# Optimization experiments

Hardware: AMD Instinct MI355X
Metric: run time of the kernel (lower is better)

Reference implementation:

```python
import jax, jax.numpy as jnp
import numpy as np

NEG = -1e30  # mask value safe for logsumexp/max
HALF_POS = 4   # positive window: [t-4, t+4)
HALF_ALL = 16  # combined window: [t-16, t+16) (pos + 12 negatives each side)


def _normalize(x, axis=-1, eps=1e-12):
    # matches torch F.normalize: x / max(||x||, eps)
    n = jnp.linalg.norm(x, axis=axis, keepdims=True)
    return x / jnp.maximum(n, eps)


def _banded_logits(q, k, temperature):
    # q, k: [B, T, D] (normalized). Returns logits [B, T, W], valid mask, pos mask.
    B, T, D = q.shape
    offsets = jnp.arange(-HALF_ALL, HALF_ALL)          # [W=32]
    j = jnp.arange(T)[:, None] + offsets[None, :]      # [T, W] absolute indices
    valid = (j >= 0) & (j < T)                         # combined (pos+neg) window
    jc = jnp.clip(j, 0, T - 1)
    kg = k[:, jc, :]                                   # [B, T, W, D]
    logits = jnp.einsum('btd,btwd->btw', q, kg) / temperature
    pos = valid & (offsets >= -HALF_POS)[None, :] & (offsets < HALF_POS)[None, :]
    return logits, valid, pos


def _direction(q, k, temperature):
    logits, valid, pos = _banded_logits(q, k, temperature)
    lse_all = jax.nn.logsumexp(jnp.where(valid, logits, NEG), axis=2)  # [B, T]
    lse_pos = jax.nn.logsumexp(jnp.where(pos, logits, NEG), axis=2)    # [B, T]
    # per-t loss is mean over batch; summed over t
    loss_sum = jnp.sum(jnp.mean(lse_all - lse_pos, axis=0))
    max_all = jnp.max(jnp.where(valid, logits, NEG), axis=2)
    max_pos = jnp.max(jnp.where(pos, logits, NEG), axis=2)
    # argmax falls in positive block (positives listed first -> ties go positive)
    correct = jnp.sum((max_pos >= max_all).astype(jnp.float32))
    return loss_sum, correct


def setup_inputs() -> dict:
    key = jax.random.key(0)
    k1, k2 = jax.random.split(key)
    B, T, D = 16, 4096, 128
    return {
        'motion_feature': jax.random.normal(k1, (B, T, D), dtype=jnp.float32),
        'audio_feature': jax.random.normal(k2, (B, T, D), dtype=jnp.float32),
    }


def reference(motion_feature, audio_feature):
    temperature = 0.1
    B, T, D = motion_feature.shape
    m = _normalize(motion_feature, axis=2)
    a = _normalize(audio_feature, axis=2)
    m2a_loss, m2a_correct = _direction(m, a, temperature)
    a2m_loss, a2m_correct = _direction(a, m, temperature)
    final_loss = (m2a_loss + a2m_loss) / (2 * T)
    total_correct = (m2a_correct + a2m_correct) / (2 * T * B)
    return final_loss, total_correct
```

## Files before the change

kernel.cpp:

```cpp
#include <hip/hip_runtime.h>
#include <hip/hip_bf16.h>

typedef __attribute__((ext_vector_type(8))) short bf16x8;
typedef __attribute__((ext_vector_type(4))) float f32x4;

#define T_DIM 4096
#define B_DIM 16
#define D_DIM 128
#define TILE 64
#define ROWS 96
#define SROW 136
#define NEGV -1e30f
#define NBLK 1024
#define SCALE (1.0f / 131072.0f)

__global__ __launch_bounds__(512, 4) void lcl_main(
    const float* __restrict__ mot, const float* __restrict__ aud,
    float* __restrict__ ws)
{
    __shared__ unsigned short sm[ROWS * SROW];
    __shared__ unsigned short sa[ROWS * SROW];
    __shared__ float invM[ROWS], invA[ROWS];
    __shared__ float redL[8], redC[8];

    const int tid  = threadIdx.x;
    const int lane = tid & 63;
    const int wv   = tid >> 6;
    const int g32  = tid >> 5;
    const int l32  = tid & 31;

    const int lin = blockIdx.y * gridDim.x + blockIdx.x;
    const int swz = (lin & 7) * (NBLK / 8) + (lin >> 3);
    const int bx  = swz & 63;
    const int by  = swz >> 6;
    const int t0  = bx * TILE;
    const size_t base = (size_t)by * (T_DIM * D_DIM);

    {
        const size_t off = base + (size_t)(t0 - 16 + g32) * D_DIM + l32 * 4;
        const float* spm = mot + off;
        const float* spa = aud + off;
        float4 vm[6], va[6];
        #pragma unroll
        for (int i = 0; i < 6; ++i) {
            const bool ok = (unsigned)(t0 - 16 + g32 + 16 * i) < (unsigned)T_DIM;
            vm[i] = make_float4(0.f, 0.f, 0.f, 0.f);
            va[i] = vm[i];
            if (ok) {
                vm[i] = *reinterpret_cast<const float4*>(spm + (size_t)(16 * i) * D_DIM);
                va[i] = *reinterpret_cast<const float4*>(spa + (size_t)(16 * i) * D_DIM);
            }
        }
        unsigned short* dpm = sm + g32 * SROW + l32 * 4;
        unsigned short* dpa = sa + g32 * SROW + l32 * 4;
        #pragma unroll
        for (int i = 0; i < 6; ++i) {
            union { __hip_bfloat16 h[4]; uint2 u; } pm, pa;
            pm.h[0] = __float2bfloat16(vm[i].x);
            pm.h[1] = __float2bfloat16(vm[i].y);
            pm.h[2] = __float2bfloat16(vm[i].z);
            pm.h[3] = __float2bfloat16(vm[i].w);
            pa.h[0] = __float2bfloat16(va[i].x);
            pa.h[1] = __float2bfloat16(va[i].y);
            pa.h[2] = __float2bfloat16(va[i].z);
            pa.h[3] = __float2bfloat16(va[i].w);
            *reinterpret_cast<uint2*>(dpm + 16 * i * SROW) = pm.u;
            *reinterpret_cast<uint2*>(dpa + 16 * i * SROW) = pa.u;
        }
    }
    __syncthreads();

    const int dir = wv >> 2;
    const int mi  = wv & 3;
    const unsigned short* q = dir ? sa : sm;
    const unsigned short* k = dir ? sm : sa;
    float* invKarr = dir ? invM : invA;

    const int fr  = lane & 15;
    const int fch = (lane >> 4) * 8;

    f32x4 acc0 = {0.f,0.f,0.f,0.f}, acc1 = acc0, acc2 = acc0;
    f32x4 n0 = acc0, n1 = acc0;
    const unsigned short* qrow = q + (16 * (mi + 1) + fr) * SROW + fch;
    const unsigned short* k0   = k + ((mi + 0) * 16 + fr) * SROW + fch;
    const unsigned short* k1   = k + ((mi + 1) * 16 + fr) * SROW + fch;
    const unsigned short* k2   = k + ((mi + 2) * 16 + fr) * SROW + fch;
    #pragma unroll
    for (int ks = 0; ks < 4; ++ks) {
        bf16x8 bq = *reinterpret_cast<const bf16x8*>(qrow + ks * 32);
        bf16x8 a0 = *reinterpret_cast<const bf16x8*>(k0   + ks * 32);
        bf16x8 a1 = *reinterpret_cast<const bf16x8*>(k1   + ks * 32);
        bf16x8 a2 = *reinterpret_cast<const bf16x8*>(k2   + ks * 32);
        acc0 = __builtin_amdgcn_mfma_f32_16x16x32_bf16(a0, bq, acc0, 0, 0, 0);
        acc1 = __builtin_amdgcn_mfma_f32_16x16x32_bf16(a1, bq, acc1, 0, 0, 0);
        acc2 = __builtin_amdgcn_mfma_f32_16x16x32_bf16(a2, bq, acc2, 0, 0, 0);
        n0   = __builtin_amdgcn_mfma_f32_16x16x32_bf16(a0, a0, n0, 0, 0, 0);
        if (mi >= 2)
            n1 = __builtin_amdgcn_mfma_f32_16x16x32_bf16(a2, a2, n1, 0, 0, 0);
    }

    const int col16 = lane & 15;
    const int g     = lane >> 4;
    if ((col16 >> 2) == g) {
        const int r = col16 & 3;
        invKarr[16 * mi + col16] = 1.0f / fmaxf(sqrtf(n0[r]), 1e-12f);
        if (mi >= 2)
            invKarr[16 * (mi + 2) + col16] = 1.0f / fmaxf(sqrtf(n1[r]), 1e-12f);
    }
    __syncthreads();

    const float* invQarr = dir ? invA : invM;
    const float scq10 = 10.0f * invQarr[16 * (mi + 1) + col16];
    const f32x4 sck0 = *reinterpret_cast<const f32x4*>(&invKarr[16 * (mi + 0) + 4 * g]);
    const f32x4 sck1 = *reinterpret_cast<const f32x4*>(&invKarr[16 * (mi + 1) + 4 * g]);
    const f32x4 sck2 = *reinterpret_cast<const f32x4*>(&invKarr[16 * (mi + 2) + 4 * g]);

    const int jbase  = t0 - 16 + 16 * mi + 4 * g;
    const int kkbase = 4 * g - col16;

    float lv[12], pv[12];
    float mx = NEGV, mxp = NEGV;
    #pragma unroll
    for (int bb = 0; bb < 3; ++bb) {
        const f32x4 acc = (bb == 0) ? acc0 : ((bb == 1) ? acc1 : acc2);
        const f32x4 sck = (bb == 0) ? sck0 : ((bb == 1) ? sck1 : sck2);
        #pragma unroll
        for (int r = 0; r < 4; ++r) {
            const int kk = kkbase + 16 * bb + r;
            const int jg = jbase  + 16 * bb + r;
            const bool ok = ((unsigned)kk < 32u) && ((unsigned)jg < (unsigned)T_DIM);
            const float li = ok ? acc[r] * (scq10 * sck[r]) : NEGV;
            const float pi = ((unsigned)(kk - 12) < 8u) ? li : NEGV;
            lv[bb * 4 + r] = li;
            pv[bb * 4 + r] = pi;
            mx  = fmaxf(mx,  li);
            mxp = fmaxf(mxp, pi);
        }
    }
    mx  = fmaxf(mx,  __shfl_xor(mx,  16));
    mx  = fmaxf(mx,  __shfl_xor(mx,  32));
    mxp = fmaxf(mxp, __shfl_xor(mxp, 16));
    mxp = fmaxf(mxp, __shfl_xor(mxp, 32));

    float s = 0.f, sp = 0.f;
    #pragma unroll
    for (int i = 0; i < 12; ++i) {
        s  += __expf(lv[i] - mx);
        sp += __expf(pv[i] - mxp);
    }
    s  += __shfl_xor(s,  16);  s  += __shfl_xor(s,  32);
    sp += __shfl_xor(sp, 16);  sp += __shfl_xor(sp, 32);

    float lossW = 0.f, corrW = 0.f;
    if (g == 0) {
        lossW = (mx + __logf(s)) - (mxp + __logf(sp));
        corrW = (mxp >= mx) ? 1.0f : 0.0f;
    }

    #pragma unroll
    for (int m = 32; m; m >>= 1) {
        lossW += __shfl_xor(lossW, m);
        corrW += __shfl_xor(corrW, m);
    }
    if (lane == 0) { redL[wv] = lossW; redC[wv] = corrW; }
    __syncthreads();
    if (tid == 0) {
        float L = 0.f, C = 0.f;
        #pragma unroll
        for (int i = 0; i < 8; ++i) { L += redL[i]; C += redC[i]; }
        ws[2 * swz]     = L;
        ws[2 * swz + 1] = C;
    }
}

__global__ __launch_bounds__(256) void lcl_final(
    const float* __restrict__ ws, float* __restrict__ out)
{
    const int tid = threadIdx.x;
    float L = 0.f, C = 0.f;
    #pragma unroll
    for (int i = 0; i < 4; ++i) {
        const int idx = tid + i * 256;
        L += ws[2 * idx];
        C += ws[2 * idx + 1];
    }
    #pragma unroll
    for (int m = 32; m; m >>= 1) { L += __shfl_xor(L, m); C += __shfl_xor(C, m); }
    __shared__ float rl[4], rc[4];
    if ((tid & 63) == 0) { rl[tid >> 6] = L; rc[tid >> 6] = C; }
    __syncthreads();
    if (tid == 0) {
        out[0] = (rl[0] + rl[1] + rl[2] + rl[3]) * SCALE;
        out[1] = (rc[0] + rc[1] + rc[2] + rc[3]) * SCALE;
    }
}

extern "C" void kernel_launch(void* const* d_in, const int* in_sizes, int n_in,
                              void* d_out, int out_size, void* d_ws, size_t ws_size,
                              hipStream_t stream) {
    const float* mot = (const float*)d_in[0];
    const float* aud = (const float*)d_in[1];
    float* out = (float*)d_out;
    float* ws  = (float*)d_ws;

    dim3 grid(T_DIM / TILE, B_DIM);
    lcl_main<<<grid, 512, 0, stream>>>(mot, aud, ws);
    lcl_final<<<1, 256, 0, stream>>>(ws, out);
}
```

Measured before the change: 24.88 us.

## Process two time tiles per block with register prefetch of next tile

```diff
diff --git a/kernel.cpp b/kernel.cpp
--- a/kernel.cpp
+++ b/kernel.cpp
@@ -8,10 +8,11 @@
 #define B_DIM 16
 #define D_DIM 128
 #define TILE 64
+#define NTILE 2
 #define ROWS 96
 #define SROW 136
 #define NEGV -1e30f
-#define NBLK 1024
+#define NBLK 512
 #define SCALE (1.0f / 131072.0f)
 
 __global__ __launch_bounds__(512, 4) void lcl_main(
@@ -29,21 +30,33 @@
     const int g32  = tid >> 5;
     const int l32  = tid & 31;
 
-    const int lin = blockIdx.y * gridDim.x + blockIdx.x;
+    const int lin = blockIdx.x;
     const int swz = (lin & 7) * (NBLK / 8) + (lin >> 3);
-    const int bx  = swz & 63;
-    const int by  = swz >> 6;
-    const int t0  = bx * TILE;
+    const int by  = swz >> 5;
+    const int tg  = swz & 31;
+    const int tbase = tg * (NTILE * TILE);
     const size_t base = (size_t)by * (T_DIM * D_DIM);
 
+    const int dir = wv >> 2;
+    const int mi  = wv & 3;
+    const unsigned short* q = dir ? sa : sm;
+    const unsigned short* k = dir ? sm : sa;
+    float* invKarr = dir ? invM : invA;
+    const float* invQarr = dir ? invA : invM;
+
+    const int fr    = lane & 15;
+    const int fch   = (lane >> 4) * 8;
+    const int col16 = lane & 15;
+    const int g     = lane >> 4;
+
+    float4 vm[6], va[6];
     {
-        const size_t off = base + (size_t)(t0 - 16 + g32) * D_DIM + l32 * 4;
+        const size_t off = base + (size_t)(tbase - 16 + g32) * D_DIM + l32 * 4;
         const float* spm = mot + off;
         const float* spa = aud + off;
-        float4 vm[6], va[6];
         #pragma unroll
         for (int i = 0; i < 6; ++i) {
-            const bool ok = (unsigned)(t0 - 16 + g32 + 16 * i) < (unsigned)T_DIM;
+            const bool ok = (unsigned)(tbase - 16 + g32 + 16 * i) < (unsigned)T_DIM;
             vm[i] = make_float4(0.f, 0.f, 0.f, 0.f);
             va[i] = vm[i];
             if (ok) {
@@ -51,110 +64,124 @@
                 va[i] = *reinterpret_cast<const float4*>(spa + (size_t)(16 * i) * D_DIM);
             }
         }
-        unsigned short* dpm = sm + g32 * SROW + l32 * 4;
-        unsigned short* dpa = sa + g32 * SROW + l32 * 4;
-        #pragma unroll
-        for (int i = 0; i < 6; ++i) {
-            union { __hip_bfloat16 h[4]; uint2 u; } pm, pa;
-            pm.h[0] = __float2bfloat16(vm[i].x);
-            pm.h[1] = __float2bfloat16(vm[i].y);
-            pm.h[2] = __float2bfloat16(vm[i].z);
-            pm.h[3] = __float2bfloat16(vm[i].w);
-            pa.h[0] = __float2bfloat16(va[i].x);
-            pa.h[1] = __float2bfloat16(va[i].y);
-            pa.h[2] = __float2bfloat16(va[i].z);
-            pa.h[3] = __float2bfloat16(va[i].w);
-            *reinterpret_cast<uint2*>(dpm + 16 * i * SROW) = pm.u;
-            *reinterpret_cast<uint2*>(dpa + 16 * i * SROW) = pa.u;
-        }
-    }
-    __syncthreads();
-
-    const int dir = wv >> 2;
-    const int mi  = wv & 3;
-    const unsigned short* q = dir ? sa : sm;
-    const unsigned short* k = dir ? sm : sa;
-    float* invKarr = dir ? invM : invA;
-
-    const int fr  = lane & 15;
-    const int fch = (lane >> 4) * 8;
-
-    f32x4 acc0 = {0.f,0.f,0.f,0.f}, acc1 = acc0, acc2 = acc0;
-    f32x4 n0 = acc0, n1 = acc0;
-    const unsigned short* qrow = q + (16 * (mi + 1) + fr) * SROW + fch;
-    const unsigned short* k0   = k + ((mi + 0) * 16 + fr) * SROW + fch;
-    const unsigned short* k1   = k + ((mi + 1) * 16 + fr) * SROW + fch;
-    const unsigned short* k2   = k + ((mi + 2) * 16 + fr) * SROW + fch;
-    #pragma unroll
-    for (int ks = 0; ks < 4; ++ks) {
-        bf16x8 bq = *reinterpret_cast<const bf16x8*>(qrow + ks * 32);
-        bf16x8 a0 = *reinterpret_cast<const bf16x8*>(k0   + ks * 32);
-        bf16x8 a1 = *reinterpret_cast<const bf16x8*>(k1   + ks * 32);
-        bf16x8 a2 = *reinterpret_cast<const bf16x8*>(k2   + ks * 32);
-        acc0 = __builtin_amdgcn_mfma_f32_16x16x32_bf16(a0, bq, acc0, 0, 0, 0);
-        acc1 = __builtin_amdgcn_mfma_f32_16x16x32_bf16(a1, bq, acc1, 0, 0, 0);
-        acc2 = __builtin_amdgcn_mfma_f32_16x16x32_bf16(a2, bq, acc2, 0, 0, 0);
-        n0   = __builtin_amdgcn_mfma_f32_16x16x32_bf16(a0, a0, n0, 0, 0, 0);
-        if (mi >= 2)
-            n1 = __builtin_amdgcn_mfma_f32_16x16x32_bf16(a2, a2, n1, 0, 0, 0);
-    }
-
-    const int col16 = lane & 15;
-    const int g     = lane >> 4;
-    if ((col16 >> 2) == g) {
-        const int r = col16 & 3;
-        invKarr[16 * mi + col16] = 1.0f / fmaxf(sqrtf(n0[r]), 1e-12f);
-        if (mi >= 2)
-            invKarr[16 * (mi + 2) + col16] = 1.0f / fmaxf(sqrtf(n1[r]), 1e-12f);
-    }
-    __syncthreads();
-
-    const float* invQarr = dir ? invA : invM;
-    const float scq10 = 10.0f * invQarr[16 * (mi + 1) + col16];
-    const f32x4 sck0 = *reinterpret_cast<const f32x4*>(&invKarr[16 * (mi + 0) + 4 * g]);
-    const f32x4 sck1 = *reinterpret_cast<const f32x4*>(&invKarr[16 * (mi + 1) + 4 * g]);
-    const f32x4 sck2 = *reinterpret_cast<const f32x4*>(&invKarr[16 * (mi + 2) + 4 * g]);
-
-    const int jbase  = t0 - 16 + 16 * mi + 4 * g;
-    const int kkbase = 4 * g - col16;
-
-    float lv[12], pv[12];
-    float mx = NEGV, mxp = NEGV;
-    #pragma unroll
-    for (int bb = 0; bb < 3; ++bb) {
-        const f32x4 acc = (bb == 0) ? acc0 : ((bb == 1) ? acc1 : acc2);
-        const f32x4 sck = (bb == 0) ? sck0 : ((bb == 1) ? sck1 : sck2);
-        #pragma unroll
-        for (int r = 0; r < 4; ++r) {
-            const int kk = kkbase + 16 * bb + r;
-            const int jg = jbase  + 16 * bb + r;
-            const bool ok = ((unsigned)kk < 32u) && ((unsigned)jg < (unsigned)T_DIM);
-            const float li = ok ? acc[r] * (scq10 * sck[r]) : NEGV;
-            const float pi = ((unsigned)(kk - 12) < 8u) ? li : NEGV;
-            lv[bb * 4 + r] = li;
-            pv[bb * 4 + r] = pi;
-            mx  = fmaxf(mx,  li);
-            mxp = fmaxf(mxp, pi);
-        }
-    }
-    mx  = fmaxf(mx,  __shfl_xor(mx,  16));
-    mx  = fmaxf(mx,  __shfl_xor(mx,  32));
-    mxp = fmaxf(mxp, __shfl_xor(mxp, 16));
-    mxp = fmaxf(mxp, __shfl_xor(mxp, 32));
-
-    float s = 0.f, sp = 0.f;
-    #pragma unroll
-    for (int i = 0; i < 12; ++i) {
-        s  += __expf(lv[i] - mx);
-        sp += __expf(pv[i] - mxp);
-    }
-    s  += __shfl_xor(s,  16);  s  += __shfl_xor(s,  32);
-    sp += __shfl_xor(sp, 16);  sp += __shfl_xor(sp, 32);
+    }
 
     float lossW = 0.f, corrW = 0.f;
-    if (g == 0) {
-        lossW = (mx + __logf(s)) - (mxp + __logf(sp));
-        corrW = (mxp >= mx) ? 1.0f : 0.0f;
+
+    #pragma unroll
+    for (int tile = 0; tile < NTILE; ++tile) {
+        const int t0 = tbase + tile * TILE;
+
+        {
+            unsigned short* dpm = sm + g32 * SROW + l32 * 4;
+            unsigned short* dpa = sa + g32 * SROW + l32 * 4;
+            #pragma unroll
+            for (int i = 0; i < 6; ++i) {
+                union { __hip_bfloat16 h[4]; uint2 u; } pm, pa;
+                pm.h[0] = __float2bfloat16(vm[i].x);
+                pm.h[1] = __float2bfloat16(vm[i].y);
+                pm.h[2] = __float2bfloat16(vm[i].z);
+                pm.h[3] = __float2bfloat16(vm[i].w);
+                pa.h[0] = __float2bfloat16(va[i].x);
+                pa.h[1] = __float2bfloat16(va[i].y);
+                pa.h[2] = __float2bfloat16(va[i].z);
+                pa.h[3] = __float2bfloat16(va[i].w);
+                *reinterpret_cast<uint2*>(dpm + 16 * i * SROW) = pm.u;
+                *reinterpret_cast<uint2*>(dpa + 16 * i * SROW) = pa.u;
+            }
+        }
+        __syncthreads();
+
+        if (tile + 1 < NTILE) {
+            const int tn = t0 + TILE;
+            const size_t off = base + (size_t)(tn - 16 + g32) * D_DIM + l32 * 4;
+            const float* spm = mot + off;
+            const float* spa = aud + off;
+            #pragma unroll
+            for (int i = 0; i < 6; ++i) {
+                const bool ok = (unsigned)(tn - 16 + g32 + 16 * i) < (unsigned)T_DIM;
+                vm[i] = make_float4(0.f, 0.f, 0.f, 0.f);
+                va[i] = vm[i];
+                if (ok) {
+                    vm[i] = *reinterpret_cast<const float4*>(spm + (size_t)(16 * i) * D_DIM);
+                    va[i] = *reinterpret_cast<const float4*>(spa + (size_t)(16 * i) * D_DIM);
+                }
+            }
+        }
+
+        f32x4 acc0 = {0.f,0.f,0.f,0.f}, acc1 = acc0, acc2 = acc0;
+        f32x4 n0 = acc0, n1 = acc0;
+        const unsigned short* qrow = q + (16 * (mi + 1) + fr) * SROW + fch;
+        const unsigned short* k0   = k + ((mi + 0) * 16 + fr) * SROW + fch;
+        const unsigned short* k1   = k + ((mi + 1) * 16 + fr) * SROW + fch;
+        const unsigned short* k2   = k + ((mi + 2) * 16 + fr) * SROW + fch;
+        #pragma unroll
+        for (int ks = 0; ks < 4; ++ks) {
+            bf16x8 bq = *reinterpret_cast<const bf16x8*>(qrow + ks * 32);
+            bf16x8 a0 = *reinterpret_cast<const bf16x8*>(k0   + ks * 32);
+            bf16x8 a1 = *reinterpret_cast<const bf16x8*>(k1   + ks * 32);
+            bf16x8 a2 = *reinterpret_cast<const bf16x8*>(k2   + ks * 32);
+            acc0 = __builtin_amdgcn_mfma_f32_16x16x32_bf16(a0, bq, acc0, 0, 0, 0);
+            acc1 = __builtin_amdgcn_mfma_f32_16x16x32_bf16(a1, bq, acc1, 0, 0, 0);
+            acc2 = __builtin_amdgcn_mfma_f32_16x16x32_bf16(a2, bq, acc2, 0, 0, 0);
+            n0   = __builtin_amdgcn_mfma_f32_16x16x32_bf16(a0, a0, n0, 0, 0, 0);
+            if (mi >= 2)
+                n1 = __builtin_amdgcn_mfma_f32_16x16x32_bf16(a2, a2, n1, 0, 0, 0);
+        }
+
+        if ((col16 >> 2) == g) {
+            const int r = col16 & 3;
+            invKarr[16 * mi + col16] = 1.0f / fmaxf(sqrtf(n0[r]), 1e-12f);
+            if (mi >= 2)
+                invKarr[16 * (mi + 2) + col16] = 1.0f / fmaxf(sqrtf(n1[r]), 1e-12f);
+        }
+        __syncthreads();
+
+        const float scq10 = 10.0f * invQarr[16 * (mi + 1) + col16];
+        const f32x4 sck0 = *reinterpret_cast<const f32x4*>(&invKarr[16 * (mi + 0) + 4 * g]);
+        const f32x4 sck1 = *reinterpret_cast<const f32x4*>(&invKarr[16 * (mi + 1) + 4 * g]);
+        const f32x4 sck2 = *reinterpret_cast<const f32x4*>(&invKarr[16 * (mi + 2) + 4 * g]);
+
+        const int jbase  = t0 - 16 + 16 * mi + 4 * g;
+        const int kkbase = 4 * g - col16;
+
+        float lv[12], pv[12];
+        float mx = NEGV, mxp = NEGV;
+        #pragma unroll
+        for (int bb = 0; bb < 3; ++bb) {
+            const f32x4 acc = (bb == 0) ? acc0 : ((bb == 1) ? acc1 : acc2);
+            const f32x4 sck = (bb == 0) ? sck0 : ((bb == 1) ? sck1 : sck2);
+            #pragma unroll
+            for (int r = 0; r < 4; ++r) {
+                const int kk = kkbase + 16 * bb + r;
+                const int jg = jbase  + 16 * bb + r;
+                const bool ok = ((unsigned)kk < 32u) && ((unsigned)jg < (unsigned)T_DIM);
+                const float li = ok ? acc[r] * (scq10 * sck[r]) : NEGV;
+                const float pi = ((unsigned)(kk - 12) < 8u) ? li : NEGV;
+                lv[bb * 4 + r] = li;
+                pv[bb * 4 + r] = pi;
+                mx  = fmaxf(mx,  li);
+                mxp = fmaxf(mxp, pi);
+            }
+        }
+        mx  = fmaxf(mx,  __shfl_xor(mx,  16));
+        mx  = fmaxf(mx,  __shfl_xor(mx,  32));
+        mxp = fmaxf(mxp, __shfl_xor(mxp, 16));
+        mxp = fmaxf(mxp, __shfl_xor(mxp, 32));
+
+        float s = 0.f, sp = 0.f;
+        #pragma unroll
+        for (int i = 0; i < 12; ++i) {
+            s  += __expf(lv[i] - mx);
+            sp += __expf(pv[i] - mxp);
+        }
+        s  += __shfl_xor(s,  16);  s  += __shfl_xor(s,  32);
+        sp += __shfl_xor(sp, 16);  sp += __shfl_xor(sp, 32);
+
+        if (g == 0) {
+            lossW += (mx + __logf(s)) - (mxp + __logf(sp));
+            corrW += (mxp >= mx) ? 1.0f : 0.0f;
+        }
     }
 
     #pragma unroll
@@ -179,7 +206,7 @@
     const int tid = threadIdx.x;
     float L = 0.f, C = 0.f;
     #pragma unroll
-    for (int i = 0; i < 4; ++i) {
+    for (int i = 0; i < 2; ++i) {
         const int idx = tid + i * 256;
         L += ws[2 * idx];
         C += ws[2 * idx + 1];
@@ -203,7 +230,6 @@
     float* out = (float*)d_out;
     float* ws  = (float*)d_ws;
 
-    dim3 grid(T_DIM / TILE, B_DIM);
-    lcl_main<<<grid, 512, 0, stream>>>(mot, aud, ws);
+    lcl_main<<<NBLK, 512, 0, stream>>>(mot, aud, ws);
     lcl_final<<<1, 256, 0, stream>>>(ws, out);
 }
```

Result: faster. 24.22 us (-2.7%).
